# Optimization experiments

Measured on AMD Instinct MI355X. Metric: run time of the kernel, lower is better.

The kernel has to match this reference:

```python
import jax, jax.numpy as jnp
from jax import lax
import numpy as np

EPS = 1e-6
GAMMA = 10.0        # interface_gamma
THRESH = 0.5        # interface_threshold
DELTA = 0.15        # boundary_delta
CG_ITERS = 20       # cg_max_iter (cg_tol=0 -> fixed iteration count, no early break)
B, S = 8, 512


def fdx(f, h):
    return (f[:, 1:, :] - f[:, :-1, :]) / h


def fdy(f, h):
    return (f[:, :, 1:] - f[:, :, :-1]) / h


def c2fx(f):
    return 0.5 * (f[:, 1:, :] + f[:, :-1, :])


def c2fy(f):
    return 0.5 * (f[:, :, 1:] + f[:, :, :-1])


def harm(c):
    # harmonic mean of cell coefficients onto x-faces [B,S-1,S] and y-faces [B,S,S-1]
    cx = 2.0 * c[:, 1:, :] * c[:, :-1, :] / (c[:, 1:, :] + c[:, :-1, :] + EPS)
    cy = 2.0 * c[:, :, 1:] * c[:, :, :-1] / (c[:, :, 1:] + c[:, :, :-1] + EPS)
    return cx, cy


def div(qx, qy, h):
    # face fluxes -> cell divergence; zero on all boundary cells
    interior = (qx[:, 1:, 1:-1] - qx[:, :-1, 1:-1]) / h + (qy[:, 1:-1, 1:] - qy[:, 1:-1, :-1]) / h
    return jnp.pad(interior, ((0, 0), (1, 1), (1, 1)))


def zb(f):
    # enforce_zero_boundary: zero out all boundary rows/cols
    return jnp.pad(f[:, 1:-1, 1:-1], ((0, 0), (1, 1), (1, 1)))


def bdot(x, y):
    return jnp.sum(x * y, axis=(1, 2))


def cgrad(f, h):
    # centered interior gradient, one-sided at edges
    gx = jnp.concatenate([(f[:, 1:2] - f[:, 0:1]) / h,
                          (f[:, 2:] - f[:, :-2]) / (2.0 * h),
                          (f[:, -1:] - f[:, -2:-1]) / h], axis=1)
    gy = jnp.concatenate([(f[:, :, 1:2] - f[:, :, 0:1]) / h,
                          (f[:, :, 2:] - f[:, :, :-2]) / (2.0 * h),
                          (f[:, :, -1:] - f[:, :, -2:-1]) / h], axis=2)
    return gx, gy


def grid_helpers(size):
    coords = np.linspace(0.0, 1.0, size)
    gx, gy = np.meshgrid(coords, coords, indexing='ij')
    d = np.minimum(np.minimum(gx, 1.0 - gx), np.minimum(gy, 1.0 - gy))
    nearest = np.argmin(np.stack([gx, 1.0 - gx, gy, 1.0 - gy], 0), axis=0)
    bnx = np.where(nearest == 0, -1.0, np.where(nearest == 1, 1.0, 0.0))
    bny = np.where(nearest == 2, -1.0, np.where(nearest == 3, 1.0, 0.0))
    xmask = np.zeros((size - 1, size)); xmask[:, 1:-1] = 1.0
    ymask = np.zeros((size, size - 1)); ymask[1:-1, :] = 1.0
    f32 = lambda a: jnp.asarray(a, jnp.float32)[None]
    return f32(d), f32(bnx), f32(bny), f32(xmask), f32(ymask)


def cg_solve(coeff, rhs, h):
    cx, cy = harm(coeff)

    def A(p):
        out = -div(cx * fdx(p, h), cy * fdy(p, h), h)
        out = out.at[:, 0, :].set(p[:, 0, :])
        out = out.at[:, -1, :].set(p[:, -1, :])
        out = out.at[:, :, 0].set(p[:, :, 0])
        out = out.at[:, :, -1].set(p[:, :, -1])
        return out

    rhs = zb(rhs)
    x = jnp.zeros_like(rhs)
    r = rhs  # A(0) == 0, including Dirichlet boundary rows of the zero field
    p = rhs
    rn = bdot(r, r)

    def step(carry, _):
        x, r, p, rn = carry
        ap = A(p)
        alpha = (rn / jnp.maximum(bdot(p, ap), EPS))[:, None, None]
        x = zb(x + alpha * p)
        r = r - alpha * ap
        nn = bdot(r, r)
        beta = (nn / jnp.maximum(rn, EPS))[:, None, None]
        p = r + beta * p
        return (x, r, p, nn), None

    (x, _, _, _), _ = lax.scan(step, (x, r, p, rn), None, length=CG_ITERS)
    return zb(x)


def forward(coeff, u_backbone, beta):
    size = coeff.shape[-1]
    h = 1.0 / float(size - 1)
    d_bdry, bnx, bny, xmask, ymask = grid_helpers(size)
    beta_bulk, beta_n, beta_t, beta_b = beta[..., 0], beta[..., 1], beta[..., 2], beta[..., 3]

    lap = div(fdx(u_backbone, h), fdy(u_backbone, h), h)
    gux, guy = fdx(u_backbone, h), fdy(u_backbone, h)
    cx, cy = harm(coeff)
    lgx, lgy = fdx(lap, h), fdy(lap, h)
    glx, gly = cgrad(jnp.log(jnp.maximum(coeff, EPS)), h)
    eta = jnp.sqrt(glx * glx + gly * gly + EPS)
    rho_int = jax.nn.sigmoid(GAMMA * (eta - THRESH))
    rho_bdry = jnp.exp(-(d_bdry * d_bdry) / (DELTA * DELTA))
    nhx, nhy = glx / eta, gly / eta  # unit interface normal; tangent = (-nhy, nhx)

    # bulk correction: higher-order flux term ~ h^2 * coeff * grad(laplacian u)
    tau_bulk_x = xmask * c2fx(beta_bulk) * (h * h) * cx * lgx
    tau_bulk_y = ymask * c2fy(beta_bulk) * (h * h) * cy * lgy
    # interface correction: normal/tangential-decomposed flux scaling near coeff jumps
    tau_int_x = xmask * c2fx(rho_int) * c2fx(beta_n * nhx - beta_t * nhy) * cx * gux
    tau_int_y = ymask * c2fy(rho_int) * c2fy(beta_n * nhy + beta_t * nhx) * cy * guy
    # boundary correction: flux scaled along outward boundary normal, decaying with distance
    tau_bdry_x = xmask * c2fx(rho_bdry) * c2fx(beta_b * bnx) * cx * gux
    tau_bdry_y = ymask * c2fy(rho_bdry) * c2fy(beta_b * bny) * cy * guy

    tau_x = tau_bulk_x + tau_int_x + tau_bdry_x
    tau_y = tau_bulk_y + tau_int_y + tau_bdry_y

    rhs = div(tau_x, tau_y, h)
    correction = cg_solve(coeff, rhs, h)
    return zb(u_backbone + correction)


def setup_inputs() -> dict:
    key = jax.random.key(0)
    k1, k2, k3 = jax.random.split(key, 3)
    coeff = jax.random.uniform(k1, (B, S, S), jnp.float32) * 2.0 + 0.5  # positive permeability
    u_backbone = jax.random.normal(k2, (B, S, S), jnp.float32) * 0.1
    beta = jax.random.normal(k3, (B, S, S, 4), jnp.float32) * 0.1
    return {"coeff": coeff, "u_backbone": u_backbone, "beta": beta}


def reference(coeff, u_backbone, beta):
    return forward(coeff, u_backbone, beta)
```

## Files before the change

### kernel.cpp

```cpp
#include <hip/hip_runtime.h>
#include <math.h>

#define S     512
#define Bsz   8
#define NCELL (S*S)
#define NTOT  (Bsz*NCELL)
#define NFACE ((S-1)*S)
#define CG_ITERS 20
#define NBLK3 512
#define TS    16

__device__ __constant__ float kINVH  = 511.0f;
__device__ __constant__ float kINV2H = 255.5f;
__device__ __constant__ float kH2    = (float)((1.0/511.0)*(1.0/511.0));

__device__ __forceinline__ void geom(int i, int j, float& rhob, float& bnx, float& bny) {
    double gx = (i == S-1) ? 1.0 : (double)i * (1.0/511.0);
    double gy = (j == S-1) ? 1.0 : (double)j * (1.0/511.0);
    double v0 = gx, v1 = 1.0 - gx, v2 = gy, v3 = 1.0 - gy;
    double m = v0; int am = 0;
    if (v1 < m) { m = v1; am = 1; }
    if (v2 < m) { m = v2; am = 2; }
    if (v3 < m) { m = v3; am = 3; }
    float d = (float)m;
    rhob = expf(-(d*d) / 0.0225f);
    bnx = (am == 0) ? -1.f : (am == 1) ? 1.f : 0.f;
    bny = (am == 2) ? -1.f : (am == 3) ? 1.f : 0.f;
}

__device__ __forceinline__ void cellfield8(const float* __restrict__ c,
                                           const float* __restrict__ uu,
                                           const float* __restrict__ bb,
                                           int i, int j, float* f) {
    int rem = i * S + j;
    float cc = c[rem];
    float uc = uu[rem];
    float lapv = 0.f;
    if (i > 0 && i < S-1 && j > 0 && j < S-1) {
        float un = uu[rem + S], us = uu[rem - S];
        float ue = uu[rem + 1], uw = uu[rem - 1];
        lapv = ((un - uc)*kINVH - (uc - us)*kINVH)*kINVH
             + ((ue - uc)*kINVH - (uc - uw)*kINVH)*kINVH;
    }
    float glx, gly;
    float lc = logf(fmaxf(cc, 1e-6f));
    if (i == 0)        { glx = (logf(fmaxf(c[rem+S],1e-6f)) - lc) * kINVH; }
    else if (i == S-1) { glx = (lc - logf(fmaxf(c[rem-S],1e-6f))) * kINVH; }
    else { glx = (logf(fmaxf(c[rem+S],1e-6f)) - logf(fmaxf(c[rem-S],1e-6f))) * kINV2H; }
    if (j == 0)        { gly = (logf(fmaxf(c[rem+1],1e-6f)) - lc) * kINVH; }
    else if (j == S-1) { gly = (lc - logf(fmaxf(c[rem-1],1e-6f))) * kINVH; }
    else { gly = (logf(fmaxf(c[rem+1],1e-6f)) - logf(fmaxf(c[rem-1],1e-6f))) * kINV2H; }
    float eta  = sqrtf(glx*glx + gly*gly + 1e-6f);
    float rhov = 1.f / (1.f + expf(-10.f * (eta - 0.5f)));
    float nhx = glx / eta, nhy = gly / eta;
    float4 b4 = ((const float4*)bb)[rem];
    f[0] = lapv; f[1] = rhov;
    f[2] = b4.y * nhx - b4.z * nhy;
    f[3] = b4.y * nhy + b4.z * nhx;
    f[4] = cc; f[5] = uc; f[6] = b4.x; f[7] = b4.w;
}

__global__ __launch_bounds__(256) void k_setup(
        const float* __restrict__ coeff, const float* __restrict__ u,
        const float* __restrict__ beta,
        float* __restrict__ taux, float* __restrict__ tauyP,
        float* __restrict__ cxP, float* __restrict__ cyP) {
    __shared__ float sF[8][TS+1][TS+8];
    int b  = blockIdx.x >> 10;
    int tl = blockIdx.x & 1023;
    int i0 = (tl >> 5) << 4;
    int j0 = (tl & 31) << 4;
    int tx = threadIdx.x & 15, ty = threadIdx.x >> 4;
    const float* cB = coeff + (b << 18);
    const float* uB = u     + (b << 18);
    const float* bB = beta  + ((size_t)b << 20);

    {   float f[8];
        cellfield8(cB, uB, bB, i0 + ty, j0 + tx, f);
        #pragma unroll
        for (int q = 0; q < 8; ++q) sF[q][ty][tx] = f[q];
    }
    if (threadIdx.x < 16 && i0 + TS < S) {
        float f[8];
        cellfield8(cB, uB, bB, i0 + TS, j0 + threadIdx.x, f);
        #pragma unroll
        for (int q = 0; q < 8; ++q) sF[q][TS][threadIdx.x] = f[q];
    }
    if (threadIdx.x >= 64 && threadIdx.x < 80 && j0 + TS < S) {
        int k = threadIdx.x - 64;
        float f[8];
        cellfield8(cB, uB, bB, i0 + k, j0 + TS, f);
        #pragma unroll
        for (int q = 0; q < 8; ++q) sF[q][k][TS] = f[q];
    }
    __syncthreads();

    int ci = i0 + ty, cj = j0 + tx;
    int rem = ci * S + cj;
    float lap0 = sF[0][ty][tx], rho0 = sF[1][ty][tx];
    float sx0  = sF[2][ty][tx], sy0  = sF[3][ty][tx];
    float c0   = sF[4][ty][tx], u0   = sF[5][ty][tx];
    float bb0  = sF[6][ty][tx], bw0  = sF[7][ty][tx];
    float rb0, nx0, ny0; geom(ci, cj, rb0, nx0, ny0);

    if (ci < S-1) {
        float lap1 = sF[0][ty+1][tx], rho1 = sF[1][ty+1][tx], sx1 = sF[2][ty+1][tx];
        float c1 = sF[4][ty+1][tx], u1 = sF[5][ty+1][tx];
        float bb1 = sF[6][ty+1][tx], bw1 = sF[7][ty+1][tx];
        float cx = 2.f * c1 * c0 / (c1 + c0 + 1e-6f);
        cxP[(b << 18) + rem] = cx;
        float t = 0.f;
        if (cj > 0 && cj < S-1) {
            float gux = (u1 - u0) * kINVH;
            float lgx = (lap1 - lap0) * kINVH;
            float rb1, nx1, ny1; geom(ci+1, cj, rb1, nx1, ny1);
            float abb  = 0.5f * (bb1 + bb0);
            float arho = 0.5f * (rho1 + rho0);
            float asx  = 0.5f * (sx1 + sx0);
            float arb  = 0.5f * (rb1 + rb0);
            float abx  = 0.5f * (bw1 * nx1 + bw0 * nx0);
            t = abb * kH2 * cx * lgx + arho * asx * cx * gux + arb * abx * cx * gux;
        }
        taux[b * NFACE + rem] = t;
    }
    if (cj < S-1) {
        float lap1 = sF[0][ty][tx+1], rho1 = sF[1][ty][tx+1], sy1 = sF[3][ty][tx+1];
        float c1 = sF[4][ty][tx+1], u1 = sF[5][ty][tx+1];
        float bb1 = sF[6][ty][tx+1], bw1 = sF[7][ty][tx+1];
        float cy = 2.f * c1 * c0 / (c1 + c0 + 1e-6f);
        cyP[(b << 18) + rem] = cy;
        float t = 0.f;
        if (ci > 0 && ci < S-1) {
            float guy = (u1 - u0) * kINVH;
            float lgy = (lap1 - lap0) * kINVH;
            float rb1, nx1, ny1; geom(ci, cj+1, rb1, nx1, ny1);
            float abb  = 0.5f * (bb1 + bb0);
            float arho = 0.5f * (rho1 + rho0);
            float asy  = 0.5f * (sy1 + sy0);
            float arb  = 0.5f * (rb1 + rb0);
            float aby  = 0.5f * (bw1 * ny1 + bw0 * ny0);
            t = abb * kH2 * cy * lgy + arho * asy * cy * guy + arb * aby * cy * guy;
        }
        tauyP[(b << 18) + rem] = t;
    }
}

__device__ __forceinline__ void load8(const float* __restrict__ src, float (&v)[8]) {
    float4 a = *(const float4*)(src);
    float4 c = *(const float4*)(src + 4);
    v[0]=a.x; v[1]=a.y; v[2]=a.z; v[3]=a.w; v[4]=c.x; v[5]=c.y; v[6]=c.z; v[7]=c.w;
}
__device__ __forceinline__ void store8(float* __restrict__ dst, const float (&v)[8]) {
    float4 a, c;
    a.x=v[0]; a.y=v[1]; a.z=v[2]; a.w=v[3];
    c.x=v[4]; c.y=v[5]; c.z=v[6]; c.w=v[7];
    *(float4*)(dst) = a;
    *(float4*)(dst + 4) = c;
}
__device__ __forceinline__ void lds_pub(float* sr, int lane, const float (&v)[8]) {
    #pragma unroll
    for (int m = 0; m < 8; ++m) sr[m*64 + lane] = v[m];
}
__device__ __forceinline__ void lds_row(const float* sr, int lane, float (&v)[8]) {
    #pragma unroll
    for (int m = 0; m < 8; ++m) v[m] = sr[m*64 + lane];
}

__device__ __forceinline__ void coh_st_row(float* rowbuf, int lane, const float (&v)[8]) {
    #pragma unroll
    for (int m = 0; m < 8; ++m)
        __hip_atomic_store(rowbuf + m*64 + lane, v[m],
                           __ATOMIC_RELAXED, __HIP_MEMORY_SCOPE_AGENT);
}
__device__ __forceinline__ void coh_ld_row(const float* rowbuf, int lane, float (&v)[8]) {
    #pragma unroll
    for (int m = 0; m < 8; ++m)
        v[m] = __hip_atomic_load(rowbuf + m*64 + lane,
                                 __ATOMIC_RELAXED, __HIP_MEMORY_SCOPE_AGENT);
}

__device__ __forceinline__ void gbar(unsigned* ctr, unsigned tgt) {
    __syncthreads();
    if (threadIdx.x == 0) {
        __hip_atomic_fetch_add(ctr, 1u, __ATOMIC_RELAXED, __HIP_MEMORY_SCOPE_AGENT);
        long g = 0;
        while (__hip_atomic_load(ctr, __ATOMIC_RELAXED, __HIP_MEMORY_SCOPE_AGENT) < tgt) {
            __builtin_amdgcn_s_sleep(2);
            if (++g > (1L << 26)) break;
        }
    }
    __syncthreads();
}

__device__ __forceinline__ void apply_stencil2(
        bool rowInt, int j0, const float (&pv)[8],
        const float (&nN)[8], const float (&nS)[8],
        const float (&cxN)[8], const float (&cxS)[8],
        const float (&cyE)[8], float cyW0, float (&apv)[8]) {
    float pW = __shfl_up(pv[7], 1);
    float pE = __shfl_down(pv[0], 1);
    #pragma unroll
    for (int m = 0; m < 8; ++m) {
        int j = j0 + m;
        if (rowInt && j >= 1 && j <= S-2) {
            float pe  = (m < 7) ? pv[m+1] : pE;
            float pw  = (m > 0) ? pv[m-1] : pW;
            float cyw = (m > 0) ? cyE[m-1] : cyW0;
            float qxp = cxN[m] * ((nN[m] - pv[m]) * kINVH);
            float qxm = cxS[m] * ((pv[m] - nS[m]) * kINVH);
            float qyp = cyE[m] * ((pe - pv[m]) * kINVH);
            float qym = cyw   * ((pv[m] - pw) * kINVH);
            apv[m] = -((qxp - qxm) * kINVH + (qyp - qym) * kINVH);
        } else {
            apv[m] = pv[m];
        }
    }
}

__global__ __launch_bounds__(512, 4) void k_cg(
        const float* __restrict__ taux, const float* __restrict__ tauy,
        const float* __restrict__ cxP,  const float* __restrict__ cyP,
        const float* __restrict__ u,    float* __restrict__ out,
        float* __restrict__ prow, double* __restrict__ dots, unsigned* bar) {
    __shared__ double red[32];
    __shared__ float srow[8][512];

    const int tid  = threadIdx.x;
    const int lane = tid & 63;
    const int w    = tid >> 6;
    const int bid  = blockIdx.x;
    const int b    = bid & 7;
    const int g    = bid >> 3;
    const int i    = (g << 3) + w;
    const int j0   = lane << 3;
    const bool rowInt = (i >= 1 && i <= S-2);
    const int base = (b << 18) + (i << 9) + j0;

    float* pubRow = prow + ((size_t)((bid << 1) | (w == 7 ? 1 : 0)) << 9);
    const bool pubEdge = (w == 0 && g > 0) || (w == 7 && g < 63);
    const float* haloS = prow + ((size_t)(((bid - 8) << 1) | 1) << 9);
    const float* haloN = prow + ((size_t)(((bid + 8) << 1) | 0) << 9);
    unsigned* ctr  = bar + (b << 4);
    double* dslot  = dots + ((size_t)((b << 6) | g) << 2);
    unsigned ph = 0;

    float cxN[8], cxS[8], cyE[8];
    float cyW0 = 0.f;
    #pragma unroll
    for (int m = 0; m < 8; ++m) { cxN[m] = 0.f; cxS[m] = 0.f; cyE[m] = 0.f; }
    if (rowInt) {
        const float* cxr = cxP + base;
        const float* cyr = cyP + base;
        load8(cxr,     cxN);
        load8(cxr - S, cxS);
        load8(cyr,     cyE);
        if (j0 > 0) cyW0 = cyr[-1];
    }

    float x[8], r[8], p[8], ap[8];
    #pragma unroll
    for (int m = 0; m < 8; ++m) { x[m]=0.f; r[m]=0.f; p[m]=0.f; ap[m]=0.f; }

    if (rowInt) {
        const float* txr = taux + b * NFACE + (i << 9) + j0;
        const float* tyr = tauy + base;
        float tx0[8], txm[8], ty0[8];
        load8(txr,     tx0);
        load8(txr - S, txm);
        load8(tyr,     ty0);
        float tyW = __shfl_up(ty0[7], 1);
        #pragma unroll
        for (int m = 0; m < 8; ++m) {
            int j = j0 + m;
            if (j >= 1 && j <= S-2) {
                float tw = (m > 0) ? ty0[m-1] : tyW;
                r[m] = (tx0[m] - txm[m]) * kINVH + (ty0[m] - tw) * kINVH;
            }
            p[m] = r[m];
        }
    }
    lds_pub(srow[w], lane, p);
    if (pubEdge) coh_st_row(pubRow, lane, p);
    ++ph; gbar(ctr, ph << 6);

    {
        float nN[8], nS[8];
        #pragma unroll
        for (int m = 0; m < 8; ++m) { nN[m] = 0.f; nS[m] = 0.f; }
        if (rowInt) {
            if (w == 0) coh_ld_row(haloS, lane, nS);
            else        lds_row(srow[w-1], lane, nS);
            if (w == 7) coh_ld_row(haloN, lane, nN);
            else        lds_row(srow[w+1], lane, nN);
        }
        apply_stencil2(rowInt, j0, p, nN, nS, cxN, cxS, cyE, cyW0, ap);
        double d0 = 0.0, d2 = 0.0, d3 = 0.0;
        #pragma unroll
        for (int m = 0; m < 8; ++m) {
            d0 += (double)p[m]  * (double)ap[m];
            d2 += (double)ap[m] * (double)ap[m];
            d3 += (double)r[m]  * (double)r[m];
        }
        #pragma unroll
        for (int off = 32; off > 0; off >>= 1) {
            d0 += __shfl_down(d0, off, 64);
            d2 += __shfl_down(d2, off, 64);
            d3 += __shfl_down(d3, off, 64);
        }
        if (lane == 0) { red[8+w] = d0; red[16+w] = d2; red[24+w] = d3; }
        __syncthreads();
        if (tid == 0) {
            double t0=0, t2=0, t3=0;
            #pragma unroll
            for (int q = 0; q < 8; ++q) { t0 += red[8+q]; t2 += red[16+q]; t3 += red[24+q]; }
            __hip_atomic_store(dslot+0, t0, __ATOMIC_RELAXED, __HIP_MEMORY_SCOPE_AGENT);
            __hip_atomic_store(dslot+1, t0, __ATOMIC_RELAXED, __HIP_MEMORY_SCOPE_AGENT);
            __hip_atomic_store(dslot+2, t2, __ATOMIC_RELAXED, __HIP_MEMORY_SCOPE_AGENT);
            __hip_atomic_store(dslot+3, t3, __ATOMIC_RELAXED, __HIP_MEMORY_SCOPE_AGENT);
        }
    }
    ++ph; gbar(ctr, ph << 6);

    double rnCur = 0.0;
    for (int it = 1; it < CG_ITERS; ++it) {
        if (w == 0) {
            const double* dr = dots + ((size_t)((b << 6) | lane) << 2);
            double s0 = __hip_atomic_load(dr+0, __ATOMIC_RELAXED, __HIP_MEMORY_SCOPE_AGENT);
            double s1 = __hip_atomic_load(dr+1, __ATOMIC_RELAXED, __HIP_MEMORY_SCOPE_AGENT);
            double s2 = __hip_atomic_load(dr+2, __ATOMIC_RELAXED, __HIP_MEMORY_SCOPE_AGENT);
            double s3 = (it == 1)
                ? __hip_atomic_load(dr+3, __ATOMIC_RELAXED, __HIP_MEMORY_SCOPE_AGENT) : 0.0;
            #pragma unroll
            for (int off = 32; off > 0; off >>= 1) {
                s0 += __shfl_down(s0, off, 64);
                s1 += __shfl_down(s1, off, 64);
                s2 += __shfl_down(s2, off, 64);
                s3 += __shfl_down(s3, off, 64);
            }
            if (lane == 0) { red[0]=s0; red[1]=s1; red[2]=s2; red[3]=s3; }
        }
        __syncthreads();
        double pap    = red[0];
        double rap    = red[1];
        double apap   = red[2];
        double rnPrev = (it == 1) ? red[3] : rnCur;
        float alphaF = (float)(rnPrev / fmax(pap, 1e-6));
        double aD = (double)alphaF;
        rnCur = rnPrev - 2.0 * aD * rap + aD * aD * apap;
        float betaF = (float)(rnCur / fmax(rnPrev, 1e-6));

        #pragma unroll
        for (int m = 0; m < 8; ++m) {
            x[m] += alphaF * p[m];
            r[m]  = r[m] - alphaF * ap[m];
            p[m]  = r[m] + betaF * p[m];
        }
        lds_pub(srow[w], lane, p);
        if (pubEdge) coh_st_row(pubRow, lane, p);
        ++ph; gbar(ctr, ph << 6);

        float nN[8], nS[8];
        #pragma unroll
        for (int m = 0; m < 8; ++m) { nN[m] = 0.f; nS[m] = 0.f; }
        if (rowInt) {
            if (w == 0) coh_ld_row(haloS, lane, nS);
            else        lds_row(srow[w-1], lane, nS);
            if (w == 7) coh_ld_row(haloN, lane, nN);
            else        lds_row(srow[w+1], lane, nN);
        }
        apply_stencil2(rowInt, j0, p, nN, nS, cxN, cxS, cyE, cyW0, ap);
        double d0 = 0.0, d1 = 0.0, d2 = 0.0;
        #pragma unroll
        for (int m = 0; m < 8; ++m) {
            d0 += (double)p[m]  * (double)ap[m];
            d1 += (double)r[m]  * (double)ap[m];
            d2 += (double)ap[m] * (double)ap[m];
        }
        #pragma unroll
        for (int off = 32; off > 0; off >>= 1) {
            d0 += __shfl_down(d0, off, 64);
            d1 += __shfl_down(d1, off, 64);
            d2 += __shfl_down(d2, off, 64);
        }
        if (lane == 0) { red[8+w] = d0; red[16+w] = d1; red[24+w] = d2; }
        __syncthreads();
        if (tid == 0) {
            double t0=0, t1=0, t2=0;
            #pragma unroll
            for (int q = 0; q < 8; ++q) { t0 += red[8+q]; t1 += red[16+q]; t2 += red[24+q]; }
            __hip_atomic_store(dslot+0, t0, __ATOMIC_RELAXED, __HIP_MEMORY_SCOPE_AGENT);
            __hip_atomic_store(dslot+1, t1, __ATOMIC_RELAXED, __HIP_MEMORY_SCOPE_AGENT);
            __hip_atomic_store(dslot+2, t2, __ATOMIC_RELAXED, __HIP_MEMORY_SCOPE_AGENT);
        }
        ++ph; gbar(ctr, ph << 6);
    }

    {
        if (w == 0) {
            const double* dr = dots + ((size_t)((b << 6) | lane) << 2);
            double s0 = __hip_atomic_load(dr+0, __ATOMIC_RELAXED, __HIP_MEMORY_SCOPE_AGENT);
            #pragma unroll
            for (int off = 32; off > 0; off >>= 1) s0 += __shfl_down(s0, off, 64);
            if (lane == 0) red[0] = s0;
        }
        __syncthreads();
        double pap = red[0];
        float alphaF = (float)(rnCur / fmax(pap, 1e-6));
        float o[8];
        #pragma unroll
        for (int m = 0; m < 8; ++m) o[m] = 0.f;
        if (rowInt) {
            float uu[8];
            load8(u + base, uu);
            #pragma unroll
            for (int m = 0; m < 8; ++m) {
                int j = j0 + m;
                if (j >= 1 && j <= S-2) o[m] = uu[m] + x[m] + alphaF * p[m];
            }
        }
        store8(out + base, o);
    }
}

extern "C" void kernel_launch(void* const* d_in, const int* in_sizes, int n_in,
                              void* d_out, int out_size, void* d_ws, size_t ws_size,
                              hipStream_t stream) {
    const float* coeff = (const float*)d_in[0];
    const float* u     = (const float*)d_in[1];
    const float* beta  = (const float*)d_in[2];
    float* out = (float*)d_out;

    float* ws    = (float*)d_ws;
    float* tauxB = ws;
    float* tauyB = ws + (size_t)NTOT;
    float* cxB   = ws + 2*(size_t)NTOT;
    float* cyB   = ws + 3*(size_t)NTOT;
    float* prow  = ws + 4*(size_t)NTOT;
    double* dots = (double*)(prow + (size_t)NBLK3*2*512);
    unsigned* bar = (unsigned*)(dots + 8*64*4);

    (void)hipMemsetAsync(bar, 0, 4096, stream);

    k_setup<<<8192, dim3(256), 0, stream>>>(coeff, u, beta, tauxB, tauyB, cxB, cyB);
    k_cg<<<NBLK3, dim3(512), 0, stream>>>(tauxB, tauyB, cxB, cyB, u, out,
                                          prow, dots, bar);
}
```

Before: 268.0 us.

## Precompute boundary geometry tables and split grid barrier into eight counters

A new small kernel precomputes the boundary distance weight and outward normals per cell, and k_setup reads them from a table instead of running the double-precision geom() three times per thread. The CG grid barrier also changes from one shared counter per batch to eight padded sub-counters. Each block increments the counter for its group, and eight threads poll all eight, with a shorter sleep. This is meant to cut atomic contention on a single address and barrier latency across the 40 barriers, at the cost of an extra launch and more polling traffic.

New measurement: 349.1 us. 1.3x slower.

```diff
diff --git a/kernel.cpp b/kernel.cpp
--- a/kernel.cpp
+++ b/kernel.cpp
@@ -26,6 +26,16 @@
     rhob = expf(-(d*d) / 0.0225f);
     bnx = (am == 0) ? -1.f : (am == 1) ? 1.f : 0.f;
     bny = (am == 2) ? -1.f : (am == 3) ? 1.f : 0.f;
+}
+
+__global__ __launch_bounds__(256) void k_geom(float* __restrict__ rbT,
+                                              float* __restrict__ bnxT,
+                                              float* __restrict__ bnyT) {
+    int t = blockIdx.x * 256 + threadIdx.x;
+    int i = t >> 9, j = t & 511;
+    float rb, nx, ny;
+    geom(i, j, rb, nx, ny);
+    rbT[t] = rb; bnxT[t] = nx; bnyT[t] = ny;
 }
 
 __device__ __forceinline__ void cellfield8(const float* __restrict__ c,
@@ -63,6 +73,8 @@
 __global__ __launch_bounds__(256) void k_setup(
         const float* __restrict__ coeff, const float* __restrict__ u,
         const float* __restrict__ beta,
+        const float* __restrict__ rbT, const float* __restrict__ bnxT,
+        const float* __restrict__ bnyT,
         float* __restrict__ taux, float* __restrict__ tauyP,
         float* __restrict__ cxP, float* __restrict__ cyP) {
     __shared__ float sF[8][TS+1][TS+8];
@@ -101,7 +113,7 @@
     float sx0  = sF[2][ty][tx], sy0  = sF[3][ty][tx];
     float c0   = sF[4][ty][tx], u0   = sF[5][ty][tx];
     float bb0  = sF[6][ty][tx], bw0  = sF[7][ty][tx];
-    float rb0, nx0, ny0; geom(ci, cj, rb0, nx0, ny0);
+    float rb0 = rbT[rem], nx0 = bnxT[rem], ny0 = bnyT[rem];
 
     if (ci < S-1) {
         float lap1 = sF[0][ty+1][tx], rho1 = sF[1][ty+1][tx], sx1 = sF[2][ty+1][tx];
@@ -113,7 +125,7 @@
         if (cj > 0 && cj < S-1) {
             float gux = (u1 - u0) * kINVH;
             float lgx = (lap1 - lap0) * kINVH;
-            float rb1, nx1, ny1; geom(ci+1, cj, rb1, nx1, ny1);
+            float rb1 = rbT[rem + S], nx1 = bnxT[rem + S];
             float abb  = 0.5f * (bb1 + bb0);
             float arho = 0.5f * (rho1 + rho0);
             float asx  = 0.5f * (sx1 + sx0);
@@ -133,7 +145,7 @@
         if (ci > 0 && ci < S-1) {
             float guy = (u1 - u0) * kINVH;
             float lgy = (lap1 - lap0) * kINVH;
-            float rb1, nx1, ny1; geom(ci, cj+1, rb1, nx1, ny1);
+            float rb1 = rbT[rem + 1], ny1 = bnyT[rem + 1];
             float abb  = 0.5f * (bb1 + bb0);
             float arho = 0.5f * (rho1 + rho0);
             float asy  = 0.5f * (sy1 + sy0);
@@ -179,13 +191,17 @@
                                  __ATOMIC_RELAXED, __HIP_MEMORY_SCOPE_AGENT);
 }
 
-__device__ __forceinline__ void gbar(unsigned* ctr, unsigned tgt) {
+__device__ __forceinline__ void gbar(unsigned* cb, int myctr, unsigned ph) {
     __syncthreads();
-    if (threadIdx.x == 0) {
-        __hip_atomic_fetch_add(ctr, 1u, __ATOMIC_RELAXED, __HIP_MEMORY_SCOPE_AGENT);
+    if (threadIdx.x == 0)
+        __hip_atomic_fetch_add(cb + (myctr << 4), 1u,
+                               __ATOMIC_RELAXED, __HIP_MEMORY_SCOPE_AGENT);
+    if (threadIdx.x < 8) {
+        unsigned tgt = ph << 3;
         long g = 0;
-        while (__hip_atomic_load(ctr, __ATOMIC_RELAXED, __HIP_MEMORY_SCOPE_AGENT) < tgt) {
-            __builtin_amdgcn_s_sleep(2);
+        while (__hip_atomic_load(cb + ((int)threadIdx.x << 4),
+                                 __ATOMIC_RELAXED, __HIP_MEMORY_SCOPE_AGENT) < tgt) {
+            __builtin_amdgcn_s_sleep(1);
             if (++g > (1L << 26)) break;
         }
     }
@@ -240,7 +256,8 @@
     const bool pubEdge = (w == 0 && g > 0) || (w == 7 && g < 63);
     const float* haloS = prow + ((size_t)(((bid - 8) << 1) | 1) << 9);
     const float* haloN = prow + ((size_t)(((bid + 8) << 1) | 0) << 9);
-    unsigned* ctr  = bar + (b << 4);
+    unsigned* cb   = bar + (b << 7);
+    const int myc  = g & 7;
     double* dslot  = dots + ((size_t)((b << 6) | g) << 2);
     unsigned ph = 0;
 
@@ -281,7 +298,7 @@
     }
     lds_pub(srow[w], lane, p);
     if (pubEdge) coh_st_row(pubRow, lane, p);
-    ++ph; gbar(ctr, ph << 6);
+    ++ph; gbar(cb, myc, ph);
 
     {
         float nN[8], nS[8];
@@ -319,7 +336,7 @@
             __hip_atomic_store(dslot+3, t3, __ATOMIC_RELAXED, __HIP_MEMORY_SCOPE_AGENT);
         }
     }
-    ++ph; gbar(ctr, ph << 6);
+    ++ph; gbar(cb, myc, ph);
 
     double rnCur = 0.0;
     for (int it = 1; it < CG_ITERS; ++it) {
@@ -357,7 +374,7 @@
         }
         lds_pub(srow[w], lane, p);
         if (pubEdge) coh_st_row(pubRow, lane, p);
-        ++ph; gbar(ctr, ph << 6);
+        ++ph; gbar(cb, myc, ph);
 
         float nN[8], nS[8];
         #pragma unroll
@@ -392,7 +409,7 @@
             __hip_atomic_store(dslot+1, t1, __ATOMIC_RELAXED, __HIP_MEMORY_SCOPE_AGENT);
             __hip_atomic_store(dslot+2, t2, __ATOMIC_RELAXED, __HIP_MEMORY_SCOPE_AGENT);
         }
-        ++ph; gbar(ctr, ph << 6);
+        ++ph; gbar(cb, myc, ph);
     }
 
     {
@@ -438,10 +455,15 @@
     float* prow  = ws + 4*(size_t)NTOT;
     double* dots = (double*)(prow + (size_t)NBLK3*2*512);
     unsigned* bar = (unsigned*)(dots + 8*64*4);
+    float* rbT   = (float*)(bar + 1024);
+    float* bnxT  = rbT + NCELL;
+    float* bnyT  = bnxT + NCELL;
 
     (void)hipMemsetAsync(bar, 0, 4096, stream);
 
-    k_setup<<<8192, dim3(256), 0, stream>>>(coeff, u, beta, tauxB, tauyB, cxB, cyB);
+    k_geom<<<1024, dim3(256), 0, stream>>>(rbT, bnxT, bnyT);
+    k_setup<<<8192, dim3(256), 0, stream>>>(coeff, u, beta, rbT, bnxT, bnyT,
+                                            tauxB, tauyB, cxB, cyB);
     k_cg<<<NBLK3, dim3(512), 0, stream>>>(tauxB, tauyB, cxB, cyB, u, out,
                                           prow, dots, bar);
 }
```

## Halve grid barriers per CG iteration by replicating halo-row recurrences locally

Applied to the files above, without the earlier changes.

Each CG iteration used to need two grid-wide barriers: one to publish p halo rows and one to publish dot products. Now edge warps keep a private copy of the neighbour block's halo p and r rows. They update these copies from the neighbour's published A·p row, which goes out with the dot products under the same barrier, so only one grid barrier per iteration remains. Dot and A·p buffers are double-buffered by parity to avoid overwrite races. This adds extra global halo traffic and floating-point recomputation of neighbour rows, which must match the neighbour's own values bit for bit.

Result: slower. 338.5 us (+26.3%).

```diff
diff --git a/kernel.cpp b/kernel.cpp
--- a/kernel.cpp
+++ b/kernel.cpp
@@ -221,7 +221,8 @@
         const float* __restrict__ taux, const float* __restrict__ tauy,
         const float* __restrict__ cxP,  const float* __restrict__ cyP,
         const float* __restrict__ u,    float* __restrict__ out,
-        float* __restrict__ prow, double* __restrict__ dots, unsigned* bar) {
+        float* __restrict__ pinit, float* __restrict__ apE,
+        double* __restrict__ dots, unsigned* bar) {
     __shared__ double red[32];
     __shared__ float srow[8][512];
 
@@ -236,12 +237,14 @@
     const bool rowInt = (i >= 1 && i <= S-2);
     const int base = (b << 18) + (i << 9) + j0;
 
-    float* pubRow = prow + ((size_t)((bid << 1) | (w == 7 ? 1 : 0)) << 9);
-    const bool pubEdge = (w == 0 && g > 0) || (w == 7 && g < 63);
-    const float* haloS = prow + ((size_t)(((bid - 8) << 1) | 1) << 9);
-    const float* haloN = prow + ((size_t)(((bid + 8) << 1) | 0) << 9);
-    unsigned* ctr  = bar + (b << 4);
-    double* dslot  = dots + ((size_t)((b << 6) | g) << 2);
+    const size_t APB = (size_t)NBLK3 * 2 * 512;
+    const size_t pubOff  = (size_t)((bid << 1) | (w == 7 ? 1 : 0)) << 9;
+    const bool isS = (w == 0 && g > 0);
+    const bool isN = (w == 7 && g < 63);
+    const bool pubEdge = isS || isN;
+    const size_t nbOff = isS ? ((size_t)(((bid - 8) << 1) | 1) << 9)
+                             : ((size_t)(((bid + 8) << 1) | 0) << 9);
+    unsigned* ctr = bar + (b << 4);
     unsigned ph = 0;
 
     float cxN[8], cxS[8], cyE[8];
@@ -257,9 +260,10 @@
         if (j0 > 0) cyW0 = cyr[-1];
     }
 
-    float x[8], r[8], p[8], ap[8];
-    #pragma unroll
-    for (int m = 0; m < 8; ++m) { x[m]=0.f; r[m]=0.f; p[m]=0.f; ap[m]=0.f; }
+    float x[8], r[8], p[8], ap[8], pN8[8], rN8[8];
+    #pragma unroll
+    for (int m = 0; m < 8; ++m) { x[m]=0.f; r[m]=0.f; p[m]=0.f; ap[m]=0.f;
+                                  pN8[m]=0.f; rN8[m]=0.f; }
 
     if (rowInt) {
         const float* txr = taux + b * NFACE + (i << 9) + j0;
@@ -280,55 +284,86 @@
         }
     }
     lds_pub(srow[w], lane, p);
-    if (pubEdge) coh_st_row(pubRow, lane, p);
+    if (pubEdge) coh_st_row(pinit + pubOff, lane, p);
     ++ph; gbar(ctr, ph << 6);
 
-    {
+    if (pubEdge) {
+        coh_ld_row(pinit + nbOff, lane, pN8);
+        for (int m = 0; m < 8; ++m) rN8[m] = pN8[m];
+    }
+
+    double rnCur = 0.0;
+    float alphaL = 0.f;
+    for (int rd = 0; rd < CG_ITERS; ++rd) {
+        const int par = rd & 1;
+        float* apPar = apE + (size_t)par * APB;
+
         float nN[8], nS[8];
         #pragma unroll
         for (int m = 0; m < 8; ++m) { nN[m] = 0.f; nS[m] = 0.f; }
         if (rowInt) {
-            if (w == 0) coh_ld_row(haloS, lane, nS);
-            else        lds_row(srow[w-1], lane, nS);
-            if (w == 7) coh_ld_row(haloN, lane, nN);
-            else        lds_row(srow[w+1], lane, nN);
+            if (w == 0) {
+                if (isS) {
+                    for (int m = 0; m < 8; ++m) nS[m] = pN8[m];
+                }
+            } else {
+                lds_row(srow[w-1], lane, nS);
+            }
+            if (w == 7) {
+                if (isN) {
+                    for (int m = 0; m < 8; ++m) nN[m] = pN8[m];
+                }
+            } else {
+                lds_row(srow[w+1], lane, nN);
+            }
         }
         apply_stencil2(rowInt, j0, p, nN, nS, cxN, cxS, cyE, cyW0, ap);
-        double d0 = 0.0, d2 = 0.0, d3 = 0.0;
+
+        double d0 = 0.0, d1 = 0.0, d2 = 0.0, d3 = 0.0;
         #pragma unroll
         for (int m = 0; m < 8; ++m) {
             d0 += (double)p[m]  * (double)ap[m];
             d2 += (double)ap[m] * (double)ap[m];
-            d3 += (double)r[m]  * (double)r[m];
+        }
+        if (rd == 0) {
+            #pragma unroll
+            for (int m = 0; m < 8; ++m) d3 += (double)r[m] * (double)r[m];
+            d1 = d0;
+        } else {
+            #pragma unroll
+            for (int m = 0; m < 8; ++m) d1 += (double)r[m] * (double)ap[m];
         }
         #pragma unroll
         for (int off = 32; off > 0; off >>= 1) {
             d0 += __shfl_down(d0, off, 64);
+            d1 += __shfl_down(d1, off, 64);
             d2 += __shfl_down(d2, off, 64);
             d3 += __shfl_down(d3, off, 64);
         }
-        if (lane == 0) { red[8+w] = d0; red[16+w] = d2; red[24+w] = d3; }
+        if (lane == 0) { red[8+w] = d0; red[16+w] = d1; red[24+w] = d2;
+                         if (rd == 0) red[w] = d3; }
         __syncthreads();
         if (tid == 0) {
-            double t0=0, t2=0, t3=0;
-            #pragma unroll
-            for (int q = 0; q < 8; ++q) { t0 += red[8+q]; t2 += red[16+q]; t3 += red[24+q]; }
-            __hip_atomic_store(dslot+0, t0, __ATOMIC_RELAXED, __HIP_MEMORY_SCOPE_AGENT);
-            __hip_atomic_store(dslot+1, t0, __ATOMIC_RELAXED, __HIP_MEMORY_SCOPE_AGENT);
-            __hip_atomic_store(dslot+2, t2, __ATOMIC_RELAXED, __HIP_MEMORY_SCOPE_AGENT);
-            __hip_atomic_store(dslot+3, t3, __ATOMIC_RELAXED, __HIP_MEMORY_SCOPE_AGENT);
-        }
-    }
-    ++ph; gbar(ctr, ph << 6);
-
-    double rnCur = 0.0;
-    for (int it = 1; it < CG_ITERS; ++it) {
+            double t0=0, t1=0, t2=0, t3=0;
+            #pragma unroll
+            for (int q = 0; q < 8; ++q) { t0 += red[8+q]; t1 += red[16+q];
+                                          t2 += red[24+q]; if (rd == 0) t3 += red[q]; }
+            double* dw = dots + ((size_t)((par << 9) + (b << 6) + g) << 2);
+            __hip_atomic_store(dw+0, t0, __ATOMIC_RELAXED, __HIP_MEMORY_SCOPE_AGENT);
+            __hip_atomic_store(dw+1, t1, __ATOMIC_RELAXED, __HIP_MEMORY_SCOPE_AGENT);
+            __hip_atomic_store(dw+2, t2, __ATOMIC_RELAXED, __HIP_MEMORY_SCOPE_AGENT);
+            if (rd == 0)
+                __hip_atomic_store(dw+3, t3, __ATOMIC_RELAXED, __HIP_MEMORY_SCOPE_AGENT);
+        }
+        if (pubEdge) coh_st_row(apPar + pubOff, lane, ap);
+        ++ph; gbar(ctr, ph << 6);
+
         if (w == 0) {
-            const double* dr = dots + ((size_t)((b << 6) | lane) << 2);
+            const double* dr = dots + ((size_t)((par << 9) + (b << 6) + lane) << 2);
             double s0 = __hip_atomic_load(dr+0, __ATOMIC_RELAXED, __HIP_MEMORY_SCOPE_AGENT);
             double s1 = __hip_atomic_load(dr+1, __ATOMIC_RELAXED, __HIP_MEMORY_SCOPE_AGENT);
             double s2 = __hip_atomic_load(dr+2, __ATOMIC_RELAXED, __HIP_MEMORY_SCOPE_AGENT);
-            double s3 = (it == 1)
+            double s3 = (rd == 0)
                 ? __hip_atomic_load(dr+3, __ATOMIC_RELAXED, __HIP_MEMORY_SCOPE_AGENT) : 0.0;
             #pragma unroll
             for (int off = 32; off > 0; off >>= 1) {
@@ -343,12 +378,14 @@
         double pap    = red[0];
         double rap    = red[1];
         double apap   = red[2];
-        double rnPrev = (it == 1) ? red[3] : rnCur;
+        double rnPrev = (rd == 0) ? red[3] : rnCur;
         float alphaF = (float)(rnPrev / fmax(pap, 1e-6));
         double aD = (double)alphaF;
         rnCur = rnPrev - 2.0 * aD * rap + aD * aD * apap;
         float betaF = (float)(rnCur / fmax(rnPrev, 1e-6));
 
+        if (rd == CG_ITERS - 1) { alphaL = alphaF; break; }
+
         #pragma unroll
         for (int m = 0; m < 8; ++m) {
             x[m] += alphaF * p[m];
@@ -356,56 +393,20 @@
             p[m]  = r[m] + betaF * p[m];
         }
         lds_pub(srow[w], lane, p);
-        if (pubEdge) coh_st_row(pubRow, lane, p);
-        ++ph; gbar(ctr, ph << 6);
-
-        float nN[8], nS[8];
-        #pragma unroll
-        for (int m = 0; m < 8; ++m) { nN[m] = 0.f; nS[m] = 0.f; }
-        if (rowInt) {
-            if (w == 0) coh_ld_row(haloS, lane, nS);
-            else        lds_row(srow[w-1], lane, nS);
-            if (w == 7) coh_ld_row(haloN, lane, nN);
-            else        lds_row(srow[w+1], lane, nN);
-        }
-        apply_stencil2(rowInt, j0, p, nN, nS, cxN, cxS, cyE, cyW0, ap);
-        double d0 = 0.0, d1 = 0.0, d2 = 0.0;
-        #pragma unroll
-        for (int m = 0; m < 8; ++m) {
-            d0 += (double)p[m]  * (double)ap[m];
-            d1 += (double)r[m]  * (double)ap[m];
-            d2 += (double)ap[m] * (double)ap[m];
-        }
-        #pragma unroll
-        for (int off = 32; off > 0; off >>= 1) {
-            d0 += __shfl_down(d0, off, 64);
-            d1 += __shfl_down(d1, off, 64);
-            d2 += __shfl_down(d2, off, 64);
-        }
-        if (lane == 0) { red[8+w] = d0; red[16+w] = d1; red[24+w] = d2; }
+
+        if (pubEdge) {
+            float apN[8];
+            coh_ld_row(apPar + nbOff, lane, apN);
+            #pragma unroll
+            for (int m = 0; m < 8; ++m) {
+                rN8[m] = rN8[m] - alphaF * apN[m];
+                pN8[m] = rN8[m] + betaF * pN8[m];
+            }
+        }
         __syncthreads();
-        if (tid == 0) {
-            double t0=0, t1=0, t2=0;
-            #pragma unroll
-            for (int q = 0; q < 8; ++q) { t0 += red[8+q]; t1 += red[16+q]; t2 += red[24+q]; }
-            __hip_atomic_store(dslot+0, t0, __ATOMIC_RELAXED, __HIP_MEMORY_SCOPE_AGENT);
-            __hip_atomic_store(dslot+1, t1, __ATOMIC_RELAXED, __HIP_MEMORY_SCOPE_AGENT);
-            __hip_atomic_store(dslot+2, t2, __ATOMIC_RELAXED, __HIP_MEMORY_SCOPE_AGENT);
-        }
-        ++ph; gbar(ctr, ph << 6);
     }
 
     {
-        if (w == 0) {
-            const double* dr = dots + ((size_t)((b << 6) | lane) << 2);
-            double s0 = __hip_atomic_load(dr+0, __ATOMIC_RELAXED, __HIP_MEMORY_SCOPE_AGENT);
-            #pragma unroll
-            for (int off = 32; off > 0; off >>= 1) s0 += __shfl_down(s0, off, 64);
-            if (lane == 0) red[0] = s0;
-        }
-        __syncthreads();
-        double pap = red[0];
-        float alphaF = (float)(rnCur / fmax(pap, 1e-6));
         float o[8];
         #pragma unroll
         for (int m = 0; m < 8; ++m) o[m] = 0.f;
@@ -415,7 +416,7 @@
             #pragma unroll
             for (int m = 0; m < 8; ++m) {
                 int j = j0 + m;
-                if (j >= 1 && j <= S-2) o[m] = uu[m] + x[m] + alphaF * p[m];
+                if (j >= 1 && j <= S-2) o[m] = uu[m] + x[m] + alphaL * p[m];
             }
         }
         store8(out + base, o);
@@ -435,13 +436,14 @@
     float* tauyB = ws + (size_t)NTOT;
     float* cxB   = ws + 2*(size_t)NTOT;
     float* cyB   = ws + 3*(size_t)NTOT;
-    float* prow  = ws + 4*(size_t)NTOT;
-    double* dots = (double*)(prow + (size_t)NBLK3*2*512);
-    unsigned* bar = (unsigned*)(dots + 8*64*4);
+    float* pinit = ws + 4*(size_t)NTOT;
+    float* apE   = pinit + (size_t)NBLK3*2*512;
+    double* dots = (double*)(apE + 2*(size_t)NBLK3*2*512);
+    unsigned* bar = (unsigned*)(dots + 2*8*64*4);
 
     (void)hipMemsetAsync(bar, 0, 4096, stream);
 
     k_setup<<<8192, dim3(256), 0, stream>>>(coeff, u, beta, tauxB, tauyB, cxB, cyB);
     k_cg<<<NBLK3, dim3(512), 0, stream>>>(tauxB, tauyB, cxB, cyB, u, out,
-                                          prow, dots, bar);
-}
+                                          pinit, apE, dots, bar);
+}
```
